# Kernel tuning notes

Hardware: AMD Instinct MI355X
Metric: run time of the kernel (lower is better)

The kernel has to match this reference:

```python
import jax, jax.numpy as jnp
import numpy as np

N, E = 10000, 30000
D_IN, E_DIM, H1, H2, C = 64, 16, 128, 64, 10


def setup_inputs() -> dict:
    key = jax.random.key(0)
    ks = jax.random.split(key, 12)
    x = jax.random.normal(ks[0], (N, D_IN), dtype=jnp.float32)
    edge_attr = jax.random.normal(ks[1], (E, E_DIM), dtype=jnp.float32)
    edge_index = jax.random.randint(ks[2], (2, E), 0, N, dtype=jnp.int64)
    # linear1: D_IN -> H1
    W1 = jax.random.normal(ks[3], (D_IN, H1), dtype=jnp.float32) / np.sqrt(D_IN)
    b1 = jnp.zeros((H1,), dtype=jnp.float32)
    # edge MLP 1: E_DIM -> H1*H2
    We1 = jax.random.normal(ks[4], (E_DIM, H1 * H2), dtype=jnp.float32) / np.sqrt(E_DIM)
    be1 = jnp.zeros((H1 * H2,), dtype=jnp.float32)
    root1 = jax.random.uniform(ks[5], (H1, H2), dtype=jnp.float32,
                               minval=-1.0 / np.sqrt(H1), maxval=1.0 / np.sqrt(H1))
    bias1 = jnp.zeros((H2,), dtype=jnp.float32)
    # edge MLP 2: E_DIM -> H2*C
    We2 = jax.random.normal(ks[6], (E_DIM, H2 * C), dtype=jnp.float32) / np.sqrt(E_DIM)
    be2 = jnp.zeros((H2 * C,), dtype=jnp.float32)
    root2 = jax.random.uniform(ks[7], (H2, C), dtype=jnp.float32,
                               minval=-1.0 / np.sqrt(H2), maxval=1.0 / np.sqrt(H2))
    bias2 = jnp.zeros((C,), dtype=jnp.float32)
    return {"x": x, "edge_attr": edge_attr, "edge_index": edge_index,
            "W1": W1, "b1": b1, "We1": We1, "be1": be1, "root1": root1, "bias1": bias1,
            "We2": We2, "be2": be2, "root2": root2, "bias2": bias2}


def _nnconv(h, src, dst, edge_attr, We, be, root, bias, c_in, c_out):
    # per-edge weight matrix from edge MLP: [E, c_in, c_out]
    W_e = (edge_attr @ We + be).reshape(-1, c_in, c_out)
    msg = jnp.einsum('ei,eio->eo', h[src], W_e)          # gather + batched matmul
    agg = jax.ops.segment_sum(msg, dst, num_segments=N)   # scatter-add to target nodes
    return agg + h @ root + bias


def reference(x, edge_attr, edge_index, W1, b1, We1, be1, root1, bias1,
              We2, be2, root2, bias2):
    src, dst = edge_index[0], edge_index[1]  # PyG: x_j = x[src], aggregate at dst
    h = jax.nn.relu(x @ W1 + b1)                               # [N, H1]
    h = jax.nn.relu(_nnconv(h, src, dst, edge_attr, We1, be1, root1, bias1, H1, H2))
    z = _nnconv(h, src, dst, edge_attr, We2, be2, root2, bias2, H2, C)
    return jax.nn.log_softmax(z, axis=1)
```

## Files before the change

kernel.cpp:

```cpp
#include <hip/hip_runtime.h>

#define N_NODES 10000
#define N_EDGES 30000
#define DIN     64
#define EDIM    16
#define H1      128
#define H2      64
#define C_OUT   10

typedef __bf16 bfrag __attribute__((ext_vector_type(8)));
typedef float  f32x4 __attribute__((ext_vector_type(4)));
typedef ushort ushort8 __attribute__((ext_vector_type(8)));

__device__ __forceinline__ ushort f2bf(float f) {
    union { float f; unsigned u; } x; x.f = f;
    unsigned r = x.u + 0x7fffu + ((x.u >> 16) & 1u);
    return (ushort)(r >> 16);
}
__device__ __forceinline__ float bf2f(ushort s) {
    union { unsigned u; float f; } x; x.u = ((unsigned)s) << 16;
    return x.f;
}

#define KA_B1   1250
#define KA_B2   (KA_B1 + 576)
#define KA_B3   (KA_B2 + 48)
#define KA_B4   (KA_B3 + 181)
__global__ __launch_bounds__(256) void kA_prep(
        const float* __restrict__ x, const float* __restrict__ W1,
        const float* __restrict__ b1,
        const float* __restrict__ We1, const float* __restrict__ root1,
        const float* __restrict__ be1,
        const float* __restrict__ We2, const float* __restrict__ be2,
        const float* __restrict__ root2,
        ushort* __restrict__ h_bf, ushort* __restrict__ B1t,
        ushort* __restrict__ B2t, float* __restrict__ aggz) {
    int t = threadIdx.x;
    int bx = blockIdx.x;
    if (bx < KA_B1) {
        __shared__ float w_lds[DIN * H1];
        __shared__ float b_lds[H1];
        __shared__ float x_lds[8][DIN];
        for (int idx = t; idx < DIN * H1 / 4; idx += 256)
            ((float4*)w_lds)[idx] = ((const float4*)W1)[idx];
        if (t < H1) b_lds[t] = b1[t];
        int n0 = bx * 8;
        if (t < 128) {
            int row = t >> 4, c4 = t & 15;
            int n = n0 + row;
            float4 v = make_float4(0.f, 0.f, 0.f, 0.f);
            if (n < N_NODES) v = ((const float4*)(x + (size_t)n * DIN))[c4];
            ((float4*)(x_lds[row]))[c4] = v;
        }
        __syncthreads();
        int nl = t >> 5;
        int o  = (t & 31) * 4;
        int n  = n0 + nl;
        float4 acc = *(const float4*)&b_lds[o];
        #pragma unroll 8
        for (int i = 0; i < DIN; ++i) {
            float xv = x_lds[nl][i];
            float4 w = *(const float4*)&w_lds[i * H1 + o];
            acc.x = fmaf(xv, w.x, acc.x);
            acc.y = fmaf(xv, w.y, acc.y);
            acc.z = fmaf(xv, w.z, acc.z);
            acc.w = fmaf(xv, w.w, acc.w);
        }
        if (n < N_NODES) {
            ushort4 s;
            s.x = f2bf(fmaxf(acc.x, 0.f));
            s.y = f2bf(fmaxf(acc.y, 0.f));
            s.z = f2bf(fmaxf(acc.z, 0.f));
            s.w = f2bf(fmaxf(acc.w, 0.f));
            *(ushort4*)&h_bf[(size_t)n * H1 + o] = s;
        }
    } else if (bx < KA_B2) {
        int idx = (bx - KA_B1) * 256 + t;
        int c = idx >> 7, i = idx & 127;
        float v;
        if (c < 1024) {
            int o = c >> 4, k = c & 15;
            v = We1[(size_t)k * (H1 * H2) + i * 64 + o];
        } else if (c < 1088) v = root1[i * 64 + (c - 1024)];
        else                 v = be1[i * 64 + (c - 1088)];
        B1t[idx] = f2bf(v);
    } else if (bx < KA_B3) {
        int idx = (bx - KA_B2) * 256 + t;
        int c = idx >> 6, j = idx & 63;
        float v = 0.f;
        if (c < 160) {
            int cc = c >> 4, k = c & 15;
            v = We2[(size_t)k * 640 + j * 10 + cc];
        }
        else if (c < 170) v = be2[j * 10 + (c - 160)];
        else if (c < 180) v = root2[j * 10 + (c - 170)];
        B2t[idx] = f2bf(v);
    } else {
        int zb = bx - KA_B3;
        for (int i = zb * 256 + t; i < 185000; i += 181 * 256)
            ((float4*)aggz)[i] = make_float4(0.f, 0.f, 0.f, 0.f);
    }
}

__global__ __launch_bounds__(256) void k3_mfma(
        const ushort* __restrict__ h_bf, const ushort* __restrict__ Bt,
        const float* __restrict__ bias1,
        ushort* __restrict__ G1t, float* __restrict__ hrb1, float* __restrict__ hb1) {
    int t = threadIdx.x;
    int wave = t >> 6, lane = t & 63;
    int quad = lane >> 4, lrow = lane & 15;
    int y = blockIdx.y;
    int nbase = blockIdx.x * 128 + wave * 32;
    int ar0 = nbase + lrow;       if (ar0 > N_NODES - 1) ar0 = N_NODES - 1;
    int ar1 = nbase + 16 + lrow;  if (ar1 > N_NODES - 1) ar1 = N_NODES - 1;
    const ushort* bbase = Bt + (size_t)y * 64 * 128;
    f32x4 acc0[4] = {}, acc1[4] = {};
    #pragma unroll
    for (int kc = 0; kc < 128; kc += 32) {
        bfrag a0 = *reinterpret_cast<const bfrag*>(h_bf + (size_t)ar0 * 128 + kc + quad * 8);
        bfrag a1 = *reinterpret_cast<const bfrag*>(h_bf + (size_t)ar1 * 128 + kc + quad * 8);
        #pragma unroll
        for (int ct = 0; ct < 4; ++ct) {
            bfrag b = *reinterpret_cast<const bfrag*>(
                bbase + (size_t)(ct * 16 + lrow) * 128 + kc + quad * 8);
            acc0[ct] = __builtin_amdgcn_mfma_f32_16x16x32_bf16(a0, b, acc0[ct], 0, 0, 0);
            acc1[ct] = __builtin_amdgcn_mfma_f32_16x16x32_bf16(a1, b, acc1[ct], 0, 0, 0);
        }
    }
    #pragma unroll
    for (int half = 0; half < 2; ++half) {
        int rbase = nbase + half * 16 + quad * 4;
        #pragma unroll
        for (int ct = 0; ct < 4; ++ct) {
            int col = ct * 16 + lrow;
            f32x4 a = half ? acc1[ct] : acc0[ct];
            #pragma unroll
            for (int r = 0; r < 4; ++r) {
                int n = rbase + r;
                if (n >= N_NODES) continue;
                float v = a[r];
                if (y < 16) {
                    G1t[(size_t)n * 1024 + y * 64 + col] = f2bf(v);
                } else if (y == 16) {
                    hrb1[(size_t)n * 64 + col] = v + bias1[col];
                } else {
                    hb1[(size_t)n * 64 + col] = v;
                }
            }
        }
    }
}

__global__ __launch_bounds__(256) void k4_edge1(
        const float* __restrict__ ea, const int* __restrict__ src_idx,
        const int* __restrict__ dst_idx, const ushort* __restrict__ G1t,
        const float* __restrict__ hb1, float* __restrict__ agg1) {
    int t = threadIdx.x;
    int e = blockIdx.x * 4 + (t >> 6);
    int o = t & 63;
    int s = src_idx[e], d = dst_idx[e];
    float m = hb1[(size_t)s * 64 + o];
    const ushort* g = G1t + (size_t)s * 1024 + o * 16;
    ushort8 g0 = *reinterpret_cast<const ushort8*>(g);
    ushort8 g1 = *reinterpret_cast<const ushort8*>(g + 8);
    const float* a = ea + (size_t)e * 16;
    #pragma unroll
    for (int k = 0; k < 8; ++k) m = fmaf(a[k], bf2f(g0[k]), m);
    #pragma unroll
    for (int k = 0; k < 8; ++k) m = fmaf(a[k + 8], bf2f(g1[k]), m);
    atomicAdd(&agg1[(size_t)d * 64 + o], m);
}

__global__ __launch_bounds__(256) void k56_mfma(
        const float* __restrict__ agg1, const float* __restrict__ hrb1,
        const ushort* __restrict__ B2t, const float* __restrict__ bias2,
        float* __restrict__ G2t, float* __restrict__ hb2, float* __restrict__ hr2) {
    int t = threadIdx.x;
    int wave = t >> 6, lane = t & 63;
    int quad = lane >> 4, lrow = lane & 15;
    int y = blockIdx.y;
    int n0 = blockIdx.x * 64 + wave * 16;
    int arow = n0 + lrow; if (arow > N_NODES - 1) arow = N_NODES - 1;
    f32x4 acc[4] = {};
    #pragma unroll
    for (int kc = 0; kc < 64; kc += 32) {
        size_t off = (size_t)arow * 64 + kc + quad * 8;
        f32x4 p0 = *(const f32x4*)(agg1 + off);
        f32x4 p1 = *(const f32x4*)(agg1 + off + 4);
        f32x4 q0 = *(const f32x4*)(hrb1 + off);
        f32x4 q1 = *(const f32x4*)(hrb1 + off + 4);
        bfrag a;
        #pragma unroll
        for (int j = 0; j < 4; ++j) {
            a[j]     = (__bf16)fmaxf(p0[j] + q0[j], 0.f);
            a[j + 4] = (__bf16)fmaxf(p1[j] + q1[j], 0.f);
        }
        #pragma unroll
        for (int ct = 0; ct < 4; ++ct) {
            bfrag b = *reinterpret_cast<const bfrag*>(
                B2t + (size_t)(y * 64 + ct * 16 + lrow) * 64 + kc + quad * 8);
            acc[ct] = __builtin_amdgcn_mfma_f32_16x16x32_bf16(a, b, acc[ct], 0, 0, 0);
        }
    }
    #pragma unroll
    for (int ct = 0; ct < 4; ++ct) {
        int cg = y * 64 + ct * 16 + lrow;
        #pragma unroll
        for (int r = 0; r < 4; ++r) {
            int n = n0 + quad * 4 + r;
            if (n >= N_NODES) continue;
            float v = acc[ct][r];
            if (cg < 160)      G2t[(size_t)n * 160 + cg] = v;
            else if (cg < 170) hb2[(size_t)n * 10 + (cg - 160)] = v;
            else if (cg < 180) hr2[(size_t)n * 10 + (cg - 170)] = v + bias2[cg - 170];
        }
    }
}

__global__ __launch_bounds__(256) void k7_edge2(
        const float* __restrict__ ea, const int* __restrict__ src_idx,
        const int* __restrict__ dst_idx, const float* __restrict__ G2t,
        const float* __restrict__ hb2, float* __restrict__ agg2) {
    int tid = blockIdx.x * 256 + threadIdx.x;
    if (tid >= N_EDGES * 10) return;
    int e = tid / 10, c = tid - e * 10;
    int s = src_idx[e], d = dst_idx[e];
    float m = hb2[(size_t)s * 10 + c];
    const float* g = G2t + (size_t)s * 160 + c * 16;
    const float* a = ea + (size_t)e * 16;
    f32x4 g0 = *(const f32x4*)g,       g1 = *(const f32x4*)(g + 4);
    f32x4 g2 = *(const f32x4*)(g + 8), g3 = *(const f32x4*)(g + 12);
    f32x4 a0 = *(const f32x4*)a,       a1 = *(const f32x4*)(a + 4);
    f32x4 a2 = *(const f32x4*)(a + 8), a3 = *(const f32x4*)(a + 12);
    #pragma unroll
    for (int k = 0; k < 4; ++k) {
        m = fmaf(a0[k], g0[k], m);
        m = fmaf(a1[k], g1[k], m);
        m = fmaf(a2[k], g2[k], m);
        m = fmaf(a3[k], g3[k], m);
    }
    atomicAdd(&agg2[(size_t)d * 10 + c], m);
}

__global__ void k8_logsoftmax(const float* __restrict__ agg2, const float* __restrict__ hr2,
                              float* __restrict__ out) {
    int n = blockIdx.x * blockDim.x + threadIdx.x;
    if (n >= N_NODES) return;
    float z[10]; float m = -1e30f;
    #pragma unroll
    for (int c = 0; c < 10; ++c) {
        z[c] = agg2[(size_t)n * 10 + c] + hr2[(size_t)n * 10 + c];
        m = fmaxf(m, z[c]);
    }
    float s = 0.f;
    #pragma unroll
    for (int c = 0; c < 10; ++c) s += expf(z[c] - m);
    float ls = logf(s);
    #pragma unroll
    for (int c = 0; c < 10; ++c) out[(size_t)n * 10 + c] = z[c] - m - ls;
}

extern "C" void kernel_launch(void* const* d_in, const int* in_sizes, int n_in,
                              void* d_out, int out_size, void* d_ws, size_t ws_size,
                              hipStream_t stream) {
    const float* x     = (const float*)d_in[0];
    const float* ea    = (const float*)d_in[1];
    const int*   eidx  = (const int*)d_in[2];
    const float* W1    = (const float*)d_in[3];
    const float* b1    = (const float*)d_in[4];
    const float* We1   = (const float*)d_in[5];
    const float* be1   = (const float*)d_in[6];
    const float* root1 = (const float*)d_in[7];
    const float* bias1 = (const float*)d_in[8];
    const float* We2   = (const float*)d_in[9];
    const float* be2   = (const float*)d_in[10];
    const float* root2 = (const float*)d_in[11];
    const float* bias2 = (const float*)d_in[12];
    float* out = (float*)d_out;

    float* ws = (float*)d_ws;
    ushort* h_bf = (ushort*)ws;
    ushort* B1t  = (ushort*)(ws + 640000);
    ushort* B2t  = (ushort*)(ws + 713728);
    ushort* G1t  = (ushort*)(ws + 719872);
    float* hrb1 = ws + 719872 + 5120000;
    float* hb1  = hrb1 + 640000;
    float* agg1 = hb1  + 640000;
    float* agg2 = agg1 + 640000;
    float* G2t  = agg2 + 100000;
    float* hb2  = G2t  + 1600000;
    float* hr2  = hb2  + 100000;

    kA_prep<<<KA_B4, 256, 0, stream>>>(x, W1, b1, We1, root1, be1, We2, be2, root2,
                                       h_bf, B1t, B2t, agg1);
    k3_mfma<<<dim3(79, 18), 256, 0, stream>>>(h_bf, B1t, bias1, G1t, hrb1, hb1);
    k4_edge1<<<7500, 256, 0, stream>>>(ea, eidx, eidx + N_EDGES, G1t, hb1, agg1);
    k56_mfma<<<dim3(157, 3), 256, 0, stream>>>(agg1, hrb1, B2t, bias2, G2t, hb2, hr2);
    k7_edge2<<<1172, 256, 0, stream>>>(ea, eidx, eidx + N_EDGES, G2t, hb2, agg2);
    k8_logsoftmax<<<40, 256, 0, stream>>>(agg2, hr2, out);
}
```

Before: 144.8 us.

## Fuse log-softmax into edge2 via last-block counter; move zeroing into k3

Log-softmax is folded into the second edge kernel: each block bumps a global counter, and the last four blocks to arrive spin until every block is done, then each handles a quarter of the nodes. This removes one kernel launch. Zeroing of agg1 and agg2, plus the counter reset, moves from the prep kernel into the k3 MFMA blocks. The first edge kernel now handles two edges per wave to increase memory-level parallelism. The spin-wait relies on all earlier blocks being resident or finishing, and it adds fence overhead.

```diff
diff --git a/kernel.cpp b/kernel.cpp
--- a/kernel.cpp
+++ b/kernel.cpp
@@ -25,7 +25,6 @@
 #define KA_B1   1250
 #define KA_B2   (KA_B1 + 576)
 #define KA_B3   (KA_B2 + 48)
-#define KA_B4   (KA_B3 + 181)
 __global__ __launch_bounds__(256) void kA_prep(
         const float* __restrict__ x, const float* __restrict__ W1,
         const float* __restrict__ b1,
@@ -34,7 +33,7 @@
         const float* __restrict__ We2, const float* __restrict__ be2,
         const float* __restrict__ root2,
         ushort* __restrict__ h_bf, ushort* __restrict__ B1t,
-        ushort* __restrict__ B2t, float* __restrict__ aggz) {
+        ushort* __restrict__ B2t) {
     int t = threadIdx.x;
     int bx = blockIdx.x;
     if (bx < KA_B1) {
@@ -84,7 +83,7 @@
         } else if (c < 1088) v = root1[i * 64 + (c - 1024)];
         else                 v = be1[i * 64 + (c - 1088)];
         B1t[idx] = f2bf(v);
-    } else if (bx < KA_B3) {
+    } else {
         int idx = (bx - KA_B2) * 256 + t;
         int c = idx >> 6, j = idx & 63;
         float v = 0.f;
@@ -95,22 +94,28 @@
         else if (c < 170) v = be2[j * 10 + (c - 160)];
         else if (c < 180) v = root2[j * 10 + (c - 170)];
         B2t[idx] = f2bf(v);
-    } else {
-        int zb = bx - KA_B3;
-        for (int i = zb * 256 + t; i < 185000; i += 181 * 256)
-            ((float4*)aggz)[i] = make_float4(0.f, 0.f, 0.f, 0.f);
     }
 }
 
 __global__ __launch_bounds__(256) void k3_mfma(
         const ushort* __restrict__ h_bf, const ushort* __restrict__ Bt,
         const float* __restrict__ bias1,
-        ushort* __restrict__ G1t, float* __restrict__ hrb1, float* __restrict__ hb1) {
+        ushort* __restrict__ G1t, float* __restrict__ hrb1, float* __restrict__ hb1,
+        float* __restrict__ agg1, float* __restrict__ agg2, unsigned* __restrict__ ctr) {
     int t = threadIdx.x;
     int wave = t >> 6, lane = t & 63;
     int quad = lane >> 4, lrow = lane & 15;
     int y = blockIdx.y;
-    int nbase = blockIdx.x * 128 + wave * 32;
+    int mx = blockIdx.x;
+    if (y == 17) {
+        for (int i = mx * 256 + t; i < 160000; i += 79 * 256)
+            ((float4*)agg1)[i] = make_float4(0.f, 0.f, 0.f, 0.f);
+    } else if (y == 16) {
+        for (int i = mx * 256 + t; i < 25000; i += 79 * 256)
+            ((float4*)agg2)[i] = make_float4(0.f, 0.f, 0.f, 0.f);
+        if (mx == 0 && t == 0) *ctr = 0u;
+    }
+    int nbase = mx * 128 + wave * 32;
     int ar0 = nbase + lrow;       if (ar0 > N_NODES - 1) ar0 = N_NODES - 1;
     int ar1 = nbase + 16 + lrow;  if (ar1 > N_NODES - 1) ar1 = N_NODES - 1;
     const ushort* bbase = Bt + (size_t)y * 64 * 128;
@@ -156,19 +161,32 @@
         const int* __restrict__ dst_idx, const ushort* __restrict__ G1t,
         const float* __restrict__ hb1, float* __restrict__ agg1) {
     int t = threadIdx.x;
-    int e = blockIdx.x * 4 + (t >> 6);
+    int e0 = blockIdx.x * 8 + (t >> 6) * 2;
     int o = t & 63;
-    int s = src_idx[e], d = dst_idx[e];
-    float m = hb1[(size_t)s * 64 + o];
-    const ushort* g = G1t + (size_t)s * 1024 + o * 16;
-    ushort8 g0 = *reinterpret_cast<const ushort8*>(g);
-    ushort8 g1 = *reinterpret_cast<const ushort8*>(g + 8);
-    const float* a = ea + (size_t)e * 16;
-    #pragma unroll
-    for (int k = 0; k < 8; ++k) m = fmaf(a[k], bf2f(g0[k]), m);
-    #pragma unroll
-    for (int k = 0; k < 8; ++k) m = fmaf(a[k + 8], bf2f(g1[k]), m);
-    atomicAdd(&agg1[(size_t)d * 64 + o], m);
+    int s0 = src_idx[e0],     d0 = dst_idx[e0];
+    int s1 = src_idx[e0 + 1], d1 = dst_idx[e0 + 1];
+    const ushort* g0p = G1t + (size_t)s0 * 1024 + o * 16;
+    const ushort* g1p = G1t + (size_t)s1 * 1024 + o * 16;
+    ushort8 ga0 = *reinterpret_cast<const ushort8*>(g0p);
+    ushort8 ga1 = *reinterpret_cast<const ushort8*>(g0p + 8);
+    ushort8 gb0 = *reinterpret_cast<const ushort8*>(g1p);
+    ushort8 gb1 = *reinterpret_cast<const ushort8*>(g1p + 8);
+    float m0 = hb1[(size_t)s0 * 64 + o];
+    float m1 = hb1[(size_t)s1 * 64 + o];
+    const float* a0 = ea + (size_t)e0 * 16;
+    const float* a1 = a0 + 16;
+    #pragma unroll
+    for (int k = 0; k < 8; ++k) {
+        m0 = fmaf(a0[k], bf2f(ga0[k]), m0);
+        m1 = fmaf(a1[k], bf2f(gb0[k]), m1);
+    }
+    #pragma unroll
+    for (int k = 0; k < 8; ++k) {
+        m0 = fmaf(a0[k + 8], bf2f(ga1[k]), m0);
+        m1 = fmaf(a1[k + 8], bf2f(gb1[k]), m1);
+    }
+    atomicAdd(&agg1[(size_t)d0 * 64 + o], m0);
+    atomicAdd(&agg1[(size_t)d1 * 64 + o], m1);
 }
 
 __global__ __launch_bounds__(256) void k56_mfma(
@@ -217,47 +235,66 @@
     }
 }
 
-__global__ __launch_bounds__(256) void k7_edge2(
+#define K78_BLOCKS 1172
+__global__ __launch_bounds__(256) void k78_edge2_softmax(
         const float* __restrict__ ea, const int* __restrict__ src_idx,
         const int* __restrict__ dst_idx, const float* __restrict__ G2t,
-        const float* __restrict__ hb2, float* __restrict__ agg2) {
-    int tid = blockIdx.x * 256 + threadIdx.x;
-    if (tid >= N_EDGES * 10) return;
-    int e = tid / 10, c = tid - e * 10;
-    int s = src_idx[e], d = dst_idx[e];
-    float m = hb2[(size_t)s * 10 + c];
-    const float* g = G2t + (size_t)s * 160 + c * 16;
-    const float* a = ea + (size_t)e * 16;
-    f32x4 g0 = *(const f32x4*)g,       g1 = *(const f32x4*)(g + 4);
-    f32x4 g2 = *(const f32x4*)(g + 8), g3 = *(const f32x4*)(g + 12);
-    f32x4 a0 = *(const f32x4*)a,       a1 = *(const f32x4*)(a + 4);
-    f32x4 a2 = *(const f32x4*)(a + 8), a3 = *(const f32x4*)(a + 12);
-    #pragma unroll
-    for (int k = 0; k < 4; ++k) {
-        m = fmaf(a0[k], g0[k], m);
-        m = fmaf(a1[k], g1[k], m);
-        m = fmaf(a2[k], g2[k], m);
-        m = fmaf(a3[k], g3[k], m);
-    }
-    atomicAdd(&agg2[(size_t)d * 10 + c], m);
-}
-
-__global__ void k8_logsoftmax(const float* __restrict__ agg2, const float* __restrict__ hr2,
-                              float* __restrict__ out) {
-    int n = blockIdx.x * blockDim.x + threadIdx.x;
-    if (n >= N_NODES) return;
-    float z[10]; float m = -1e30f;
-    #pragma unroll
-    for (int c = 0; c < 10; ++c) {
-        z[c] = agg2[(size_t)n * 10 + c] + hr2[(size_t)n * 10 + c];
-        m = fmaxf(m, z[c]);
-    }
-    float s = 0.f;
-    #pragma unroll
-    for (int c = 0; c < 10; ++c) s += expf(z[c] - m);
-    float ls = logf(s);
-    #pragma unroll
-    for (int c = 0; c < 10; ++c) out[(size_t)n * 10 + c] = z[c] - m - ls;
+        const float* __restrict__ hb2, const float* __restrict__ hr2,
+        float* __restrict__ agg2, unsigned* __restrict__ ctr,
+        float* __restrict__ out) {
+    int t = threadIdx.x;
+    int tid = blockIdx.x * 256 + t;
+    if (tid < N_EDGES * 10) {
+        int e = tid / 10, c = tid - e * 10;
+        int s = src_idx[e], d = dst_idx[e];
+        float m = hb2[(size_t)s * 10 + c];
+        const float* g = G2t + (size_t)s * 160 + c * 16;
+        const float* a = ea + (size_t)e * 16;
+        f32x4 g0 = *(const f32x4*)g,       g1 = *(const f32x4*)(g + 4);
+        f32x4 g2 = *(const f32x4*)(g + 8), g3 = *(const f32x4*)(g + 12);
+        f32x4 a0 = *(const f32x4*)a,       a1 = *(const f32x4*)(a + 4);
+        f32x4 a2 = *(const f32x4*)(a + 8), a3 = *(const f32x4*)(a + 12);
+        #pragma unroll
+        for (int k = 0; k < 4; ++k) {
+            m = fmaf(a0[k], g0[k], m);
+            m = fmaf(a1[k], g1[k], m);
+            m = fmaf(a2[k], g2[k], m);
+            m = fmaf(a3[k], g3[k], m);
+        }
+        atomicAdd(&agg2[(size_t)d * 10 + c], m);
+    }
+    __shared__ unsigned prev_s;
+    __syncthreads();
+    if (t == 0) {
+        __builtin_amdgcn_fence(__ATOMIC_RELEASE, "agent");
+        prev_s = atomicAdd(ctr, 1u);
+    }
+    __syncthreads();
+    unsigned prev = prev_s;
+    if (prev < K78_BLOCKS - 4) return;
+    if (t == 0) {
+        while (__hip_atomic_load(ctr, __ATOMIC_RELAXED, __HIP_MEMORY_SCOPE_AGENT)
+               < K78_BLOCKS)
+            __builtin_amdgcn_s_sleep(8);
+        __builtin_amdgcn_fence(__ATOMIC_ACQUIRE, "agent");
+    }
+    __syncthreads();
+    int slice = prev - (K78_BLOCKS - 4);
+    int nlo = slice * 2500, nhi = nlo + 2500;
+    for (int n = nlo + t; n < nhi; n += 256) {
+        float z[10]; float mx = -1e30f;
+        #pragma unroll
+        for (int c = 0; c < 10; ++c) {
+            z[c] = agg2[(size_t)n * 10 + c] + hr2[(size_t)n * 10 + c];
+            mx = fmaxf(mx, z[c]);
+        }
+        float s = 0.f;
+        #pragma unroll
+        for (int c = 0; c < 10; ++c) s += expf(z[c] - mx);
+        float ls = logf(s);
+        #pragma unroll
+        for (int c = 0; c < 10; ++c) out[(size_t)n * 10 + c] = z[c] - mx - ls;
+    }
 }
 
 extern "C" void kernel_launch(void* const* d_in, const int* in_sizes, int n_in,
@@ -290,12 +327,14 @@
     float* G2t  = agg2 + 100000;
     float* hb2  = G2t  + 1600000;
     float* hr2  = hb2  + 100000;
-
-    kA_prep<<<KA_B4, 256, 0, stream>>>(x, W1, b1, We1, root1, be1, We2, be2, root2,
-                                       h_bf, B1t, B2t, agg1);
-    k3_mfma<<<dim3(79, 18), 256, 0, stream>>>(h_bf, B1t, bias1, G1t, hrb1, hb1);
-    k4_edge1<<<7500, 256, 0, stream>>>(ea, eidx, eidx + N_EDGES, G1t, hb1, agg1);
+    unsigned* ctr = (unsigned*)(hr2 + 100000);
+
+    kA_prep<<<KA_B3, 256, 0, stream>>>(x, W1, b1, We1, root1, be1, We2, be2, root2,
+                                       h_bf, B1t, B2t);
+    k3_mfma<<<dim3(79, 18), 256, 0, stream>>>(h_bf, B1t, bias1, G1t, hrb1, hb1,
+                                              agg1, agg2, ctr);
+    k4_edge1<<<3750, 256, 0, stream>>>(ea, eidx, eidx + N_EDGES, G1t, hb1, agg1);
     k56_mfma<<<dim3(157, 3), 256, 0, stream>>>(agg1, hrb1, B2t, bias2, G2t, hb2, hr2);
-    k7_edge2<<<1172, 256, 0, stream>>>(ea, eidx, eidx + N_EDGES, G2t, hb2, agg2);
-    k8_logsoftmax<<<40, 256, 0, stream>>>(agg2, hr2, out);
-}
+    k78_edge2_softmax<<<K78_BLOCKS, 256, 0, stream>>>(ea, eidx, eidx + N_EDGES,
+                                                      G2t, hb2, hr2, agg2, ctr, out);
+}
```

Measured after the change: 189.1 us. 1.31x slower.
